# Kernel tuning notes

Measured on AMD Instinct MI355X. Metric: run time of the kernel, lower is better.

## Reference

```python
import jax, jax.numpy as jnp
import numpy as np

N_VERTS = 1_000_000
N_EDGES = 3_000_000
H, W = 1024, 1024
MAX_DEPTH = 10.0
DEPTH_SCALE = 1.0
CREGU = 2000.0


def setup_inputs() -> dict:
    key = jax.random.key(0)
    k1, k2, k3, k4, k5, k6 = jax.random.split(key, 6)
    # mesh vertices roughly in a unit-radius blob
    vertices = jax.random.normal(k1, (N_VERTS, 3), dtype=jnp.float32) * 0.5
    vertices_ref = vertices + 0.01 * jax.random.normal(k2, (N_VERTS, 3), dtype=jnp.float32)
    quaternion = jax.random.normal(k3, (4,), dtype=jnp.float32) + jnp.array([0., 0., 0., 1.], jnp.float32)
    translation = jax.random.normal(k4, (3,), dtype=jnp.float32) * 0.05
    hand_image = jax.random.uniform(k5, (H, W), dtype=jnp.float32) * MAX_DEPTH
    # camera per MeshDepthFitterEnergy.setImage: R = diag(1,-1,-1), focal = 2*W
    object_center = np.zeros(3, np.float32)
    object_radius = 0.5
    camera_center = object_center + np.array([-0.5, 0.0, 5.0], np.float32) * object_radius
    R = np.array([[1., 0., 0.], [0., -1., 0.], [0., 0., -1.]], np.float32)
    T = -R.T.dot(camera_center)
    focal = 2.0 * W
    intrinsic = jnp.array([[focal, 0., W / 2.], [0., focal, H / 2.], [0., 0., 1.]], jnp.float32)
    extrinsic = jnp.array(np.column_stack((R, T)), jnp.float32)
    edges = jax.random.randint(k6, (N_EDGES, 2), 0, N_VERTS, dtype=jnp.int64)
    return {"vertices": vertices, "vertices_ref": vertices_ref, "quaternion": quaternion,
            "translation": translation, "hand_image": hand_image,
            "intrinsic": intrinsic, "extrinsic": extrinsic, "edges": edges}


def _qrot(q, v):
    # q: [4] (x,y,z,w) normalized; v: [N,3]
    qvec = q[:3]
    uv = jnp.cross(jnp.broadcast_to(qvec, v.shape), v)
    uuv = jnp.cross(jnp.broadcast_to(qvec, v.shape), uv)
    return v + 2.0 * (q[3] * uv + uuv)


def _forward(vertices, vertices_ref, quaternion, translation, hand_image,
             intrinsic, extrinsic, edges):
    # rigid transform
    q = quaternion / jnp.linalg.norm(quaternion)
    v_centered = vertices - jnp.mean(vertices, axis=0, keepdims=True)
    v_t = _qrot(q, v_centered) + translation  # [N,3]
    # camera projection: P_cam = R x + T ; pix = K P_cam / z
    p_cam = v_t @ extrinsic[:, :3].T + extrinsic[:, 3]  # [N,3]
    proj = p_cam @ intrinsic.T
    z = p_cam[:, 2] * DEPTH_SCALE
    u = proj[:, 0] / proj[:, 2]
    v = proj[:, 1] / proj[:, 2]
    xi = jnp.clip(jnp.round(u), 0, W - 1).astype(jnp.int32)
    yi = jnp.clip(jnp.round(v), 0, H - 1).astype(jnp.int32)
    flat = yi * W + xi  # [N]
    # z-buffer: scatter-min of per-vertex depth (invalid/behind-camera -> MAX_DEPTH)
    zvalid = jnp.where(z > 0, z, MAX_DEPTH)
    depth_flat = jnp.full((H * W,), MAX_DEPTH, dtype=vertices.dtype).at[flat].min(zvalid)
    depth = jnp.clip(depth_flat, 0.0, MAX_DEPTH).reshape(H, W)
    diff_image = (depth - hand_image) ** 2
    e_data = jnp.sum(diff_image)
    # Laplacian rigid energy: cregu * || L (V - Vref) ||^2 over the edge graph
    dv = vertices - vertices_ref
    src, dst = edges[:, 0], edges[:, 1]
    deg = jax.ops.segment_sum(jnp.ones((N_EDGES,), vertices.dtype), src, num_segments=N_VERTS)
    neigh = jax.ops.segment_sum(dv[dst], src, num_segments=N_VERTS)  # [N,3]
    ldv = deg[:, None] * dv - neigh
    e_rigid = CREGU * jnp.sum(ldv ** 2)
    return e_data + e_rigid


def reference(vertices, vertices_ref, quaternion, translation, hand_image,
              intrinsic, extrinsic, edges):
    return _forward(vertices, vertices_ref, quaternion, translation, hand_image,
                    intrinsic, extrinsic, edges)
```

## Files before the change

### kernel.cpp

```cpp
#include <hip/hip_runtime.h>

#define W_IMG 1024
#define H_IMG 1024
#define HW_IMG (W_IMG * H_IMG)
#define NV 1000000
#define NE 3000000
#define NV4 (NE / 2)
#define MAX_DEPTH 10.0f
#define CREGU 2000.0f

#define NBUCKET 245
#define BSHIFT 12
#define BSIZE 4096
#define CAPSHIFT 14
#define CAP (1 << CAPSHIFT)

#define PREP_BLOCKS 2048
#define SCAT_V4 2048
#define SCAT_EDGES (SCAT_V4 * 2)
#define SCAT_BLOCKS ((NV4 + SCAT_V4 - 1) / SCAT_V4)
#define GEO_BLOCKS 2048
#define TSIZE 1024
#define EB 1024
#define EDATA_BLOCKS 64

#define QXY 4096.0f
#define IQXY 2.44140625e-4f
#define QZ 2048.0f
#define IQZ 4.8828125e-4f
#define BXY2 1024
#define BZ2 512

typedef int v4i __attribute__((ext_vector_type(4)));
typedef unsigned v4u __attribute__((ext_vector_type(4)));

__device__ __forceinline__ unsigned pack_dv32(float x, float y, float z) {
    x = fminf(fmaxf(x, -0.2f), 0.2f);
    y = fminf(fmaxf(y, -0.2f), 0.2f);
    z = fminf(fmaxf(z, -0.2f), 0.2f);
    unsigned px = (unsigned)((int)rintf(x * QXY) + BXY2);
    unsigned py = (unsigned)((int)rintf(y * QXY) + BXY2);
    unsigned pz = (unsigned)((int)rintf(z * QZ) + BZ2);
    return (px << 21) | (py << 10) | pz;
}

__device__ __forceinline__ unsigned long long expand_dv(unsigned p) {
    unsigned long long x = (p >> 21) & 0x7FFu;
    unsigned long long y = (p >> 10) & 0x7FFu;
    unsigned long long z = p & 0x3FFu;
    return (x << 44) | (y << 24) | (z << 6) | 1ull;
}

__device__ __forceinline__ float block_sum(float v, float* smem) {
#pragma unroll
    for (int o = 32; o > 0; o >>= 1) v += __shfl_down(v, o, 64);
    int lane = threadIdx.x & 63;
    int wid  = threadIdx.x >> 6;
    int nw   = blockDim.x >> 6;
    if (lane == 0) smem[wid] = v;
    __syncthreads();
    float r = 0.f;
    if (threadIdx.x == 0)
        for (int w = 0; w < nw; ++w) r += smem[w];
    __syncthreads();
    return r;
}

__device__ __forceinline__ void prefix245_fast(const unsigned* __restrict__ src,
                                               unsigned* dst, unsigned* wtmp) {
    int t = threadIdx.x;
    int lane = t & 63, wid = t >> 6;
    unsigned h = (t < NBUCKET) ? src[t] : 0u;
    unsigned incl = h;
#pragma unroll
    for (int o = 1; o < 64; o <<= 1) {
        unsigned v = __shfl_up(incl, o, 64);
        if (lane >= o) incl += v;
    }
    if (lane == 63) wtmp[wid] = incl;
    __syncthreads();
    unsigned woff = 0u;
    if (wid > 0) woff += wtmp[0];
    if (wid > 1) woff += wtmp[1];
    if (wid > 2) woff += wtmp[2];
    dst[t] = woff + incl - h;
    __syncthreads();
}

struct ScatSM {
    unsigned sort[SCAT_EDGES];
    unsigned char sBin[SCAT_EDGES];
    unsigned sLh[NBUCKET];
    unsigned sPfx[256];
    unsigned sDelta[256];
    unsigned wtmp[4];
};

__global__ void k_prep(const float* __restrict__ verts,
                       const float* __restrict__ verts_ref,
                       unsigned* __restrict__ pdv32,
                       unsigned* __restrict__ depth_bits, int ncd,
                       unsigned long long* __restrict__ neigh, int modeA,
                       const v4i* __restrict__ edges2,
                       unsigned* __restrict__ rec32,
                       unsigned* __restrict__ reserve,
                       float4* __restrict__ partial) {
    __shared__ float smem[4];
    __shared__ ScatSM sc;

    if (blockIdx.x < SCAT_BLOCKS) {
        if (!modeA) return;
        int base = blockIdx.x * SCAT_V4;
        for (int t = threadIdx.x; t < NBUCKET; t += blockDim.x) sc.sLh[t] = 0u;
        __syncthreads();

        v4i e[8];
        unsigned r0[8], r1[8];
#pragma unroll
        for (int k = 0; k < 8; ++k) {
            int idx = base + k * 256 + (int)threadIdx.x;
            if (idx < NV4) {
                e[k] = __builtin_nontemporal_load(&edges2[idx]);
                r0[k] = atomicAdd(&sc.sLh[(unsigned)e[k].x >> BSHIFT], 1u);
                r1[k] = atomicAdd(&sc.sLh[(unsigned)e[k].z >> BSHIFT], 1u);
            }
        }
        __syncthreads();
        prefix245_fast(sc.sLh, sc.sPfx, sc.wtmp);
        for (int t = threadIdx.x; t < NBUCKET; t += blockDim.x) {
            unsigned c = sc.sLh[t];
            unsigned res = c ? atomicAdd(&reserve[t], c) : 0u;
            sc.sDelta[t] = ((unsigned)t << CAPSHIFT) + res - sc.sPfx[t];
        }
#pragma unroll
        for (int k = 0; k < 8; ++k) {
            int idx = base + k * 256 + (int)threadIdx.x;
            if (idx < NV4) {
                unsigned s0 = (unsigned)e[k].x;
                unsigned b0 = s0 >> BSHIFT;
                unsigned slot0 = sc.sPfx[b0] + r0[k];
                sc.sort[slot0] = ((unsigned)e[k].y << 12) | (s0 & (BSIZE - 1));
                sc.sBin[slot0] = (unsigned char)b0;
                unsigned s1 = (unsigned)e[k].z;
                unsigned b1 = s1 >> BSHIFT;
                unsigned slot1 = sc.sPfx[b1] + r1[k];
                sc.sort[slot1] = ((unsigned)e[k].w << 12) | (s1 & (BSIZE - 1));
                sc.sBin[slot1] = (unsigned char)b1;
            }
        }
        __syncthreads();
        int nrec = (base + SCAT_V4 <= NV4) ? SCAT_EDGES : 2 * (NV4 - base);
#pragma unroll
        for (int k = 0; k < 16; ++k) {
            int t = k * 256 + (int)threadIdx.x;
            if (t < nrec) {
                unsigned r = sc.sort[t];
                unsigned b = sc.sBin[t];
                unsigned g = t + sc.sDelta[b];
                if (g - ((unsigned)b << CAPSHIFT) < CAP)
                    rec32[g] = r;
            }
        }
        return;
    }

    int sid = blockIdx.x - SCAT_BLOCKS;
    int i = sid * blockDim.x + threadIdx.x;
    int stride = PREP_BLOCKS * blockDim.x;

    float sx = 0.f, sy = 0.f, sz = 0.f;
    for (int j = i; j < NV; j += stride) {
        float x = verts[3 * j + 0];
        float y = verts[3 * j + 1];
        float z = verts[3 * j + 2];
        sx += x; sy += y; sz += z;
        pdv32[j] = pack_dv32(x - verts_ref[3 * j + 0],
                             y - verts_ref[3 * j + 1],
                             z - verts_ref[3 * j + 2]);
        if (!modeA) neigh[j] = 0ull;
    }

    size_t totd4 = (size_t)ncd * (HW_IMG / 4);
    v4u dinit;
    dinit.x = dinit.y = dinit.z = dinit.w = 0x41200000u;
    for (size_t j = i; j < totd4; j += stride) ((v4u*)depth_bits)[j] = dinit;

    float bx = block_sum(sx, smem);
    float by = block_sum(sy, smem);
    float bz = block_sum(sz, smem);
    if (threadIdx.x == 0) {
        float4 p; p.x = bx; p.y = by; p.z = bz; p.w = 0.f;
        partial[sid] = p;
    }
}

__global__ void k_main(const v4i* __restrict__ edges2,
                       const unsigned* __restrict__ pdv32,
                       unsigned long long* __restrict__ neigh,
                       const float* __restrict__ verts,
                       const float* __restrict__ quat,
                       const float* __restrict__ trans,
                       const float* __restrict__ intr,
                       const float* __restrict__ extr,
                       const float4* __restrict__ partial,
                       unsigned* __restrict__ depth_bits, int ncd) {
    __shared__ struct {
        unsigned h_key[TSIZE];
        unsigned h_val[TSIZE];
        float rsm[8];
    } sm;

    if (blockIdx.x >= GEO_BLOCKS) {
        int sb = blockIdx.x - GEO_BLOCKS;
        int base = sb * SCAT_V4;
#pragma unroll
        for (int k = 0; k < 8; ++k) {
            int idx = base + k * 256 + (int)threadIdx.x;
            if (idx < NV4) {
                v4i e = __builtin_nontemporal_load(&edges2[idx]);
                atomicAdd(&neigh[(size_t)(unsigned)e.x], expand_dv(pdv32[e.y]));
                atomicAdd(&neigh[(size_t)(unsigned)e.z], expand_dv(pdv32[e.w]));
            }
        }
        return;
    }

    int gb = blockIdx.x;
    for (int s = threadIdx.x; s < TSIZE; s += blockDim.x) {
        sm.h_key[s] = 0xFFFFFFFFu;
        sm.h_val[s] = 0xFFFFFFFFu;
    }
    __syncthreads();

    float sx = 0.f, sy = 0.f, sz = 0.f;
    for (int p = threadIdx.x; p < PREP_BLOCKS; p += blockDim.x) {
        float4 v = partial[p];
        sx += v.x; sy += v.y; sz += v.z;
    }
    float bx = block_sum(sx, sm.rsm);
    float by = block_sum(sy, sm.rsm);
    float bz = block_sum(sz, sm.rsm);
    if (threadIdx.x == 0) {
        const float inv_nv = 1.0f / (float)NV;
        sm.rsm[4] = bx * inv_nv;
        sm.rsm[5] = by * inv_nv;
        sm.rsm[6] = bz * inv_nv;
    }
    __syncthreads();
    float mx = sm.rsm[4], my = sm.rsm[5], mz = sm.rsm[6];

    float qx = quat[0], qy = quat[1], qz = quat[2], qw = quat[3];
    float qn = rsqrtf(qx * qx + qy * qy + qz * qz + qw * qw);
    qx *= qn; qy *= qn; qz *= qn; qw *= qn;
    float t0 = trans[0], t1 = trans[1], t2 = trans[2];
    float e0 = extr[0], e1 = extr[1], e2 = extr[2],  e3 = extr[3];
    float e4 = extr[4], e5 = extr[5], e6 = extr[6],  e7 = extr[7];
    float e8 = extr[8], e9 = extr[9], e10 = extr[10], e11 = extr[11];
    float i0 = intr[0], i1 = intr[1], i2 = intr[2];
    float i3 = intr[3], i4 = intr[4], i5 = intr[5];
    float i6 = intr[6], i7 = intr[7], i8 = intr[8];

    unsigned* __restrict__ db = depth_bits + (size_t)(gb & (ncd - 1)) * HW_IMG;

    int stride = GEO_BLOCKS * blockDim.x;
    for (int j = gb * blockDim.x + threadIdx.x; j < NV; j += stride) {
        float vx = __builtin_nontemporal_load(&verts[3 * j + 0]) - mx;
        float vy = __builtin_nontemporal_load(&verts[3 * j + 1]) - my;
        float vz = __builtin_nontemporal_load(&verts[3 * j + 2]) - mz;

        float uvx = qy * vz - qz * vy;
        float uvy = qz * vx - qx * vz;
        float uvz = qx * vy - qy * vx;
        float uuvx = qy * uvz - qz * uvy;
        float uuvy = qz * uvx - qx * uvz;
        float uuvz = qx * uvy - qy * uvx;
        float tx = vx + 2.f * (qw * uvx + uuvx) + t0;
        float ty = vy + 2.f * (qw * uvy + uuvy) + t1;
        float tz = vz + 2.f * (qw * uvz + uuvz) + t2;

        float px = e0 * tx + e1 * ty + e2  * tz + e3;
        float py = e4 * tx + e5 * ty + e6  * tz + e7;
        float pz = e8 * tx + e9 * ty + e10 * tz + e11;

        float pr0 = i0 * px + i1 * py + i2 * pz;
        float pr1 = i3 * px + i4 * py + i5 * pz;
        float pr2 = i6 * px + i7 * py + i8 * pz;

        float u = pr0 / pr2;
        float v = pr1 / pr2;
        float ru = rintf(u);
        float rv = rintf(v);
        bool border = (ru < 0.f) | (ru > (float)(W_IMG - 1)) |
                      (rv < 0.f) | (rv > (float)(H_IMG - 1));
        float xf = fminf(fmaxf(ru, 0.f), (float)(W_IMG - 1));
        float yf = fminf(fmaxf(rv, 0.f), (float)(H_IMG - 1));
        unsigned flat = (unsigned)((int)yf * W_IMG + (int)xf);

        if (pz > 0.f) {
            unsigned zbits = __float_as_uint(pz);
            bool direct = !border;
            if (border) {
                unsigned slot = (flat * 2654435761u) >> 22;
                bool done = false;
#pragma unroll
                for (int p = 0; p < 4; ++p) {
                    unsigned old = atomicCAS(&sm.h_key[slot], 0xFFFFFFFFu, flat);
                    if (old == 0xFFFFFFFFu || old == flat) {
                        atomicMin(&sm.h_val[slot], zbits);
                        done = true;
                        break;
                    }
                    slot = (slot + 1) & (TSIZE - 1);
                }
                direct = !done;
            }
            if (direct) atomicMin(&db[flat], zbits);
        }
    }
    __syncthreads();
    for (int s = threadIdx.x; s < TSIZE; s += blockDim.x) {
        unsigned k = sm.h_key[s];
        if (k != 0xFFFFFFFFu) atomicMin(&db[k], sm.h_val[s]);
    }
}

__global__ __launch_bounds__(EB, 2)
void k_energy(const unsigned* __restrict__ depth_bits, int ncd,
              const float* __restrict__ hand,
              const unsigned* __restrict__ pdv32,
              const unsigned* __restrict__ rec32,
              const unsigned* __restrict__ reserve,
              const unsigned long long* __restrict__ neigh, int modeA,
              float* out) {
    __shared__ unsigned long long acc[BSIZE];
    __shared__ float smem[16];

    if (blockIdx.x < NBUCKET) {
        int b = blockIdx.x;
        int vbase = b * BSIZE;
        int nvert = (NV - vbase < BSIZE) ? (NV - vbase) : BSIZE;
        if (modeA) {
            unsigned count = reserve[b];
            if (count > CAP) count = CAP;
            const unsigned* rb = rec32 + ((size_t)b << CAPSHIFT);
            for (int v = threadIdx.x; v < BSIZE; v += blockDim.x) acc[v] = 0ull;
            __syncthreads();
            unsigned i = threadIdx.x;
            for (; i + 3u * EB < count; i += 4u * EB) {
                unsigned q0 = rb[i];
                unsigned q1 = rb[i + EB];
                unsigned q2 = rb[i + 2u * EB];
                unsigned q3 = rb[i + 3u * EB];
                unsigned p0 = pdv32[q0 >> 12];
                unsigned p1 = pdv32[q1 >> 12];
                unsigned p2 = pdv32[q2 >> 12];
                unsigned p3 = pdv32[q3 >> 12];
                atomicAdd(&acc[q0 & (BSIZE - 1u)], expand_dv(p0));
                atomicAdd(&acc[q1 & (BSIZE - 1u)], expand_dv(p1));
                atomicAdd(&acc[q2 & (BSIZE - 1u)], expand_dv(p2));
                atomicAdd(&acc[q3 & (BSIZE - 1u)], expand_dv(p3));
            }
            for (; i < count; i += EB) {
                unsigned q = rb[i];
                atomicAdd(&acc[q & (BSIZE - 1u)], expand_dv(pdv32[q >> 12]));
            }
            __syncthreads();
        }
        float lacc = 0.f;
        for (int v = threadIdx.x; v < nvert; v += blockDim.x) {
            unsigned long long n = modeA ? acc[v] : neigh[(size_t)vbase + v];
            int cnt = (int)(n & 63ull);
            int rz  = (int)((n >> 6)  & 0x3FFFFull);
            int ry  = (int)((n >> 24) & 0xFFFFFull);
            int rx  = (int)(n >> 44);
            float nx = (float)(rx - cnt * BXY2) * IQXY;
            float ny = (float)(ry - cnt * BXY2) * IQXY;
            float nz = (float)(rz - cnt * BZ2)  * IQZ;
            unsigned p = pdv32[vbase + v];
            float dx = (float)((int)((p >> 21) & 0x7FFu) - BXY2) * IQXY;
            float dy = (float)((int)((p >> 10) & 0x7FFu) - BXY2) * IQXY;
            float dz = (float)((int)(p & 0x3FFu) - BZ2) * IQZ;
            float dg = (float)cnt;
            float lx = dg * dx - nx;
            float ly = dg * dy - ny;
            float lz = dg * dz - nz;
            lacc += lx * lx + ly * ly + lz * lz;
        }
        float bsum = block_sum(lacc, smem);
        if (threadIdx.x == 0) atomicAdd(out, CREGU * bsum);
    } else {
        int eb = blockIdx.x - NBUCKET;
        int i = eb * blockDim.x + threadIdx.x;
        int stride = EDATA_BLOCKS * blockDim.x;
        float accd = 0.f;
        const int nq = HW_IMG / 4;
        for (int j = i; j < nq; j += stride) {
            v4u d0 = ((const v4u*)depth_bits)[j];
            float m0 = __uint_as_float(d0.x);
            float m1 = __uint_as_float(d0.y);
            float m2 = __uint_as_float(d0.z);
            float m3 = __uint_as_float(d0.w);
            for (int c = 1; c < ncd; ++c) {
                v4u dc = ((const v4u*)(depth_bits + (size_t)c * HW_IMG))[j];
                m0 = fminf(m0, __uint_as_float(dc.x));
                m1 = fminf(m1, __uint_as_float(dc.y));
                m2 = fminf(m2, __uint_as_float(dc.z));
                m3 = fminf(m3, __uint_as_float(dc.w));
            }
            const float* hp = hand + 4 * (size_t)j;
            float f0 = fminf(fmaxf(m0, 0.f), MAX_DEPTH) - hp[0];
            float f1 = fminf(fmaxf(m1, 0.f), MAX_DEPTH) - hp[1];
            float f2 = fminf(fmaxf(m2, 0.f), MAX_DEPTH) - hp[2];
            float f3 = fminf(fmaxf(m3, 0.f), MAX_DEPTH) - hp[3];
            accd += f0 * f0 + f1 * f1 + f2 * f2 + f3 * f3;
        }
        float bsum = block_sum(accd, smem);
        if (threadIdx.x == 0) atomicAdd(out, bsum);
    }
}

extern "C" void kernel_launch(void* const* d_in, const int* in_sizes, int n_in,
                              void* d_out, int out_size, void* d_ws, size_t ws_size,
                              hipStream_t stream) {
    const float* verts     = (const float*)d_in[0];
    const float* verts_ref = (const float*)d_in[1];
    const float* quat      = (const float*)d_in[2];
    const float* trans     = (const float*)d_in[3];
    const float* hand      = (const float*)d_in[4];
    const float* intr      = (const float*)d_in[5];
    const float* extr      = (const float*)d_in[6];
    const int*   edges     = (const int*)d_in[7];
    float* out = (float*)d_out;

    char* ws = (char*)d_ws;
    const size_t OFF_BINS = (size_t)NV * 4;
    const size_t OFF_PART = OFF_BINS + 4096;
    const size_t OFF_REC  = OFF_PART + (size_t)PREP_BLOCKS * 16;

    const size_t A_FIX = OFF_REC + ((size_t)NBUCKET << CAPSHIFT) * 4;
    const size_t B_FIX = OFF_REC + (size_t)NV * 8;

    int modeA, ncd;
    size_t OFF_DEPTH;
    if (ws_size >= A_FIX + 4ull * HW_IMG * 4)      { modeA = 1; ncd = 4; OFF_DEPTH = A_FIX; }
    else if (ws_size >= A_FIX + 2ull * HW_IMG * 4) { modeA = 1; ncd = 2; OFF_DEPTH = A_FIX; }
    else if (ws_size >= A_FIX + 1ull * HW_IMG * 4) { modeA = 1; ncd = 1; OFF_DEPTH = A_FIX; }
    else if (ws_size >= B_FIX + 4ull * HW_IMG * 4) { modeA = 0; ncd = 4; OFF_DEPTH = B_FIX; }
    else if (ws_size >= B_FIX + 2ull * HW_IMG * 4) { modeA = 0; ncd = 2; OFF_DEPTH = B_FIX; }
    else                                           { modeA = 0; ncd = 1; OFF_DEPTH = B_FIX; }

    unsigned*           pdv32      = (unsigned*)ws;
    unsigned*           hist       = (unsigned*)(ws + OFF_BINS);
    unsigned*           reserve    = hist + 256;
    float4*             partial    = (float4*)(ws + OFF_PART);
    unsigned*           rec32      = (unsigned*)(ws + OFF_REC);
    unsigned long long* neigh      = (unsigned long long*)(ws + OFF_REC);
    unsigned*           depth_bits = (unsigned*)(ws + OFF_DEPTH);

    const int B = 256;

    hipMemsetAsync(ws + OFF_BINS, 0, 4096, stream);
    hipMemsetAsync(d_out, 0, sizeof(float), stream);

    k_prep<<<SCAT_BLOCKS + PREP_BLOCKS, B, 0, stream>>>(
        verts, verts_ref, pdv32, depth_bits, ncd, neigh, modeA,
        (const v4i*)edges, rec32, reserve, partial);
    k_main<<<modeA ? GEO_BLOCKS : (GEO_BLOCKS + SCAT_BLOCKS), B, 0, stream>>>(
        (const v4i*)edges, pdv32, neigh,
        verts, quat, trans, intr, extr, partial, depth_bits, ncd);
    k_energy<<<NBUCKET + EDATA_BLOCKS, EB, 0, stream>>>(
        depth_bits, ncd, hand, pdv32, rec32, reserve, neigh, modeA, out);
}
```

Before: 214.7 us.

## Move bucketed neighbor accumulation into geometry kernel to overlap with rasterization

After: 201.5 us. 1.07x faster.

```diff
diff --git a/kernel.cpp b/kernel.cpp
--- a/kernel.cpp
+++ b/kernel.cpp
@@ -23,6 +23,7 @@
 #define TSIZE 1024
 #define EB 1024
 #define EDATA_BLOCKS 64
+#define EDATA_BLOCKS_A 128
 
 #define QXY 4096.0f
 #define IQXY 2.44140625e-4f
@@ -194,8 +195,22 @@
     }
 }
 
+union MainSM {
+    struct {
+        unsigned h_key[TSIZE];
+        unsigned h_val[TSIZE];
+        float rsm[8];
+    } geo;
+    struct {
+        unsigned long long acc[BSIZE];
+        float smem[4];
+    } bk;
+};
+
 __global__ void k_main(const v4i* __restrict__ edges2,
                        const unsigned* __restrict__ pdv32,
+                       const unsigned* __restrict__ rec32,
+                       const unsigned* __restrict__ reserve,
                        unsigned long long* __restrict__ neigh,
                        const float* __restrict__ verts,
                        const float* __restrict__ quat,
@@ -203,172 +218,42 @@
                        const float* __restrict__ intr,
                        const float* __restrict__ extr,
                        const float4* __restrict__ partial,
-                       unsigned* __restrict__ depth_bits, int ncd) {
-    __shared__ struct {
-        unsigned h_key[TSIZE];
-        unsigned h_val[TSIZE];
-        float rsm[8];
-    } sm;
-
-    if (blockIdx.x >= GEO_BLOCKS) {
-        int sb = blockIdx.x - GEO_BLOCKS;
-        int base = sb * SCAT_V4;
-#pragma unroll
-        for (int k = 0; k < 8; ++k) {
-            int idx = base + k * 256 + (int)threadIdx.x;
-            if (idx < NV4) {
-                v4i e = __builtin_nontemporal_load(&edges2[idx]);
-                atomicAdd(&neigh[(size_t)(unsigned)e.x], expand_dv(pdv32[e.y]));
-                atomicAdd(&neigh[(size_t)(unsigned)e.z], expand_dv(pdv32[e.w]));
-            }
-        }
-        return;
-    }
-
-    int gb = blockIdx.x;
-    for (int s = threadIdx.x; s < TSIZE; s += blockDim.x) {
-        sm.h_key[s] = 0xFFFFFFFFu;
-        sm.h_val[s] = 0xFFFFFFFFu;
-    }
-    __syncthreads();
-
-    float sx = 0.f, sy = 0.f, sz = 0.f;
-    for (int p = threadIdx.x; p < PREP_BLOCKS; p += blockDim.x) {
-        float4 v = partial[p];
-        sx += v.x; sy += v.y; sz += v.z;
-    }
-    float bx = block_sum(sx, sm.rsm);
-    float by = block_sum(sy, sm.rsm);
-    float bz = block_sum(sz, sm.rsm);
-    if (threadIdx.x == 0) {
-        const float inv_nv = 1.0f / (float)NV;
-        sm.rsm[4] = bx * inv_nv;
-        sm.rsm[5] = by * inv_nv;
-        sm.rsm[6] = bz * inv_nv;
-    }
-    __syncthreads();
-    float mx = sm.rsm[4], my = sm.rsm[5], mz = sm.rsm[6];
-
-    float qx = quat[0], qy = quat[1], qz = quat[2], qw = quat[3];
-    float qn = rsqrtf(qx * qx + qy * qy + qz * qz + qw * qw);
-    qx *= qn; qy *= qn; qz *= qn; qw *= qn;
-    float t0 = trans[0], t1 = trans[1], t2 = trans[2];
-    float e0 = extr[0], e1 = extr[1], e2 = extr[2],  e3 = extr[3];
-    float e4 = extr[4], e5 = extr[5], e6 = extr[6],  e7 = extr[7];
-    float e8 = extr[8], e9 = extr[9], e10 = extr[10], e11 = extr[11];
-    float i0 = intr[0], i1 = intr[1], i2 = intr[2];
-    float i3 = intr[3], i4 = intr[4], i5 = intr[5];
-    float i6 = intr[6], i7 = intr[7], i8 = intr[8];
-
-    unsigned* __restrict__ db = depth_bits + (size_t)(gb & (ncd - 1)) * HW_IMG;
-
-    int stride = GEO_BLOCKS * blockDim.x;
-    for (int j = gb * blockDim.x + threadIdx.x; j < NV; j += stride) {
-        float vx = __builtin_nontemporal_load(&verts[3 * j + 0]) - mx;
-        float vy = __builtin_nontemporal_load(&verts[3 * j + 1]) - my;
-        float vz = __builtin_nontemporal_load(&verts[3 * j + 2]) - mz;
-
-        float uvx = qy * vz - qz * vy;
-        float uvy = qz * vx - qx * vz;
-        float uvz = qx * vy - qy * vx;
-        float uuvx = qy * uvz - qz * uvy;
-        float uuvy = qz * uvx - qx * uvz;
-        float uuvz = qx * uvy - qy * uvx;
-        float tx = vx + 2.f * (qw * uvx + uuvx) + t0;
-        float ty = vy + 2.f * (qw * uvy + uuvy) + t1;
-        float tz = vz + 2.f * (qw * uvz + uuvz) + t2;
-
-        float px = e0 * tx + e1 * ty + e2  * tz + e3;
-        float py = e4 * tx + e5 * ty + e6  * tz + e7;
-        float pz = e8 * tx + e9 * ty + e10 * tz + e11;
-
-        float pr0 = i0 * px + i1 * py + i2 * pz;
-        float pr1 = i3 * px + i4 * py + i5 * pz;
-        float pr2 = i6 * px + i7 * py + i8 * pz;
-
-        float u = pr0 / pr2;
-        float v = pr1 / pr2;
-        float ru = rintf(u);
-        float rv = rintf(v);
-        bool border = (ru < 0.f) | (ru > (float)(W_IMG - 1)) |
-                      (rv < 0.f) | (rv > (float)(H_IMG - 1));
-        float xf = fminf(fmaxf(ru, 0.f), (float)(W_IMG - 1));
-        float yf = fminf(fmaxf(rv, 0.f), (float)(H_IMG - 1));
-        unsigned flat = (unsigned)((int)yf * W_IMG + (int)xf);
-
-        if (pz > 0.f) {
-            unsigned zbits = __float_as_uint(pz);
-            bool direct = !border;
-            if (border) {
-                unsigned slot = (flat * 2654435761u) >> 22;
-                bool done = false;
-#pragma unroll
-                for (int p = 0; p < 4; ++p) {
-                    unsigned old = atomicCAS(&sm.h_key[slot], 0xFFFFFFFFu, flat);
-                    if (old == 0xFFFFFFFFu || old == flat) {
-                        atomicMin(&sm.h_val[slot], zbits);
-                        done = true;
-                        break;
-                    }
-                    slot = (slot + 1) & (TSIZE - 1);
-                }
-                direct = !done;
-            }
-            if (direct) atomicMin(&db[flat], zbits);
-        }
-    }
-    __syncthreads();
-    for (int s = threadIdx.x; s < TSIZE; s += blockDim.x) {
-        unsigned k = sm.h_key[s];
-        if (k != 0xFFFFFFFFu) atomicMin(&db[k], sm.h_val[s]);
-    }
-}
-
-__global__ __launch_bounds__(EB, 2)
-void k_energy(const unsigned* __restrict__ depth_bits, int ncd,
-              const float* __restrict__ hand,
-              const unsigned* __restrict__ pdv32,
-              const unsigned* __restrict__ rec32,
-              const unsigned* __restrict__ reserve,
-              const unsigned long long* __restrict__ neigh, int modeA,
-              float* out) {
-    __shared__ unsigned long long acc[BSIZE];
-    __shared__ float smem[16];
-
-    if (blockIdx.x < NBUCKET) {
+                       unsigned* __restrict__ depth_bits, int ncd,
+                       int nb, float* __restrict__ out) {
+    __shared__ MainSM sm;
+
+    if ((int)blockIdx.x < nb) {
         int b = blockIdx.x;
         int vbase = b * BSIZE;
         int nvert = (NV - vbase < BSIZE) ? (NV - vbase) : BSIZE;
-        if (modeA) {
-            unsigned count = reserve[b];
-            if (count > CAP) count = CAP;
-            const unsigned* rb = rec32 + ((size_t)b << CAPSHIFT);
-            for (int v = threadIdx.x; v < BSIZE; v += blockDim.x) acc[v] = 0ull;
-            __syncthreads();
-            unsigned i = threadIdx.x;
-            for (; i + 3u * EB < count; i += 4u * EB) {
-                unsigned q0 = rb[i];
-                unsigned q1 = rb[i + EB];
-                unsigned q2 = rb[i + 2u * EB];
-                unsigned q3 = rb[i + 3u * EB];
-                unsigned p0 = pdv32[q0 >> 12];
-                unsigned p1 = pdv32[q1 >> 12];
-                unsigned p2 = pdv32[q2 >> 12];
-                unsigned p3 = pdv32[q3 >> 12];
-                atomicAdd(&acc[q0 & (BSIZE - 1u)], expand_dv(p0));
-                atomicAdd(&acc[q1 & (BSIZE - 1u)], expand_dv(p1));
-                atomicAdd(&acc[q2 & (BSIZE - 1u)], expand_dv(p2));
-                atomicAdd(&acc[q3 & (BSIZE - 1u)], expand_dv(p3));
-            }
-            for (; i < count; i += EB) {
-                unsigned q = rb[i];
-                atomicAdd(&acc[q & (BSIZE - 1u)], expand_dv(pdv32[q >> 12]));
-            }
-            __syncthreads();
-        }
+        unsigned count = reserve[b];
+        if (count > CAP) count = CAP;
+        const unsigned* rb = rec32 + ((size_t)b << CAPSHIFT);
+        for (int v = threadIdx.x; v < BSIZE; v += blockDim.x) sm.bk.acc[v] = 0ull;
+        __syncthreads();
+        unsigned i = threadIdx.x;
+        for (; i + 768u < count; i += 1024u) {
+            unsigned q0 = rb[i];
+            unsigned q1 = rb[i + 256u];
+            unsigned q2 = rb[i + 512u];
+            unsigned q3 = rb[i + 768u];
+            unsigned p0 = pdv32[q0 >> 12];
+            unsigned p1 = pdv32[q1 >> 12];
+            unsigned p2 = pdv32[q2 >> 12];
+            unsigned p3 = pdv32[q3 >> 12];
+            atomicAdd(&sm.bk.acc[q0 & (BSIZE - 1u)], expand_dv(p0));
+            atomicAdd(&sm.bk.acc[q1 & (BSIZE - 1u)], expand_dv(p1));
+            atomicAdd(&sm.bk.acc[q2 & (BSIZE - 1u)], expand_dv(p2));
+            atomicAdd(&sm.bk.acc[q3 & (BSIZE - 1u)], expand_dv(p3));
+        }
+        for (; i < count; i += 256u) {
+            unsigned q = rb[i];
+            atomicAdd(&sm.bk.acc[q & (BSIZE - 1u)], expand_dv(pdv32[q >> 12]));
+        }
+        __syncthreads();
         float lacc = 0.f;
         for (int v = threadIdx.x; v < nvert; v += blockDim.x) {
-            unsigned long long n = modeA ? acc[v] : neigh[(size_t)vbase + v];
+            unsigned long long n = sm.bk.acc[v];
             int cnt = (int)(n & 63ull);
             int rz  = (int)((n >> 6)  & 0x3FFFFull);
             int ry  = (int)((n >> 24) & 0xFFFFFull);
@@ -386,12 +271,164 @@
             float lz = dg * dz - nz;
             lacc += lx * lx + ly * ly + lz * lz;
         }
+        float bsum = block_sum(lacc, sm.bk.smem);
+        if (threadIdx.x == 0) atomicAdd(out, CREGU * bsum);
+        return;
+    }
+
+    int gb = blockIdx.x - nb;
+    if (gb >= GEO_BLOCKS) {
+        int sb = gb - GEO_BLOCKS;
+        int base = sb * SCAT_V4;
+#pragma unroll
+        for (int k = 0; k < 8; ++k) {
+            int idx = base + k * 256 + (int)threadIdx.x;
+            if (idx < NV4) {
+                v4i e = __builtin_nontemporal_load(&edges2[idx]);
+                atomicAdd(&neigh[(size_t)(unsigned)e.x], expand_dv(pdv32[e.y]));
+                atomicAdd(&neigh[(size_t)(unsigned)e.z], expand_dv(pdv32[e.w]));
+            }
+        }
+        return;
+    }
+
+    for (int s = threadIdx.x; s < TSIZE; s += blockDim.x) {
+        sm.geo.h_key[s] = 0xFFFFFFFFu;
+        sm.geo.h_val[s] = 0xFFFFFFFFu;
+    }
+    __syncthreads();
+
+    float sx = 0.f, sy = 0.f, sz = 0.f;
+    for (int p = threadIdx.x; p < PREP_BLOCKS; p += blockDim.x) {
+        float4 v = partial[p];
+        sx += v.x; sy += v.y; sz += v.z;
+    }
+    float bx = block_sum(sx, sm.geo.rsm);
+    float by = block_sum(sy, sm.geo.rsm);
+    float bz = block_sum(sz, sm.geo.rsm);
+    if (threadIdx.x == 0) {
+        const float inv_nv = 1.0f / (float)NV;
+        sm.geo.rsm[4] = bx * inv_nv;
+        sm.geo.rsm[5] = by * inv_nv;
+        sm.geo.rsm[6] = bz * inv_nv;
+    }
+    __syncthreads();
+    float mx = sm.geo.rsm[4], my = sm.geo.rsm[5], mz = sm.geo.rsm[6];
+
+    float qx = quat[0], qy = quat[1], qz = quat[2], qw = quat[3];
+    float qn = rsqrtf(qx * qx + qy * qy + qz * qz + qw * qw);
+    qx *= qn; qy *= qn; qz *= qn; qw *= qn;
+    float t0 = trans[0], t1 = trans[1], t2 = trans[2];
+    float e0 = extr[0], e1 = extr[1], e2 = extr[2],  e3 = extr[3];
+    float e4 = extr[4], e5 = extr[5], e6 = extr[6],  e7 = extr[7];
+    float e8 = extr[8], e9 = extr[9], e10 = extr[10], e11 = extr[11];
+    float i0 = intr[0], i1 = intr[1], i2 = intr[2];
+    float i3 = intr[3], i4 = intr[4], i5 = intr[5];
+    float i6 = intr[6], i7 = intr[7], i8 = intr[8];
+
+    unsigned* __restrict__ db = depth_bits + (size_t)(gb & (ncd - 1)) * HW_IMG;
+
+    int stride = GEO_BLOCKS * blockDim.x;
+    for (int j = gb * blockDim.x + threadIdx.x; j < NV; j += stride) {
+        float vx = __builtin_nontemporal_load(&verts[3 * j + 0]) - mx;
+        float vy = __builtin_nontemporal_load(&verts[3 * j + 1]) - my;
+        float vz = __builtin_nontemporal_load(&verts[3 * j + 2]) - mz;
+
+        float uvx = qy * vz - qz * vy;
+        float uvy = qz * vx - qx * vz;
+        float uvz = qx * vy - qy * vx;
+        float uuvx = qy * uvz - qz * uvy;
+        float uuvy = qz * uvx - qx * uvz;
+        float uuvz = qx * uvy - qy * uvx;
+        float tx = vx + 2.f * (qw * uvx + uuvx) + t0;
+        float ty = vy + 2.f * (qw * uvy + uuvy) + t1;
+        float tz = vz + 2.f * (qw * uvz + uuvz) + t2;
+
+        float px = e0 * tx + e1 * ty + e2  * tz + e3;
+        float py = e4 * tx + e5 * ty + e6  * tz + e7;
+        float pz = e8 * tx + e9 * ty + e10 * tz + e11;
+
+        float pr0 = i0 * px + i1 * py + i2 * pz;
+        float pr1 = i3 * px + i4 * py + i5 * pz;
+        float pr2 = i6 * px + i7 * py + i8 * pz;
+
+        float u = pr0 / pr2;
+        float v = pr1 / pr2;
+        float ru = rintf(u);
+        float rv = rintf(v);
+        bool border = (ru < 0.f) | (ru > (float)(W_IMG - 1)) |
+                      (rv < 0.f) | (rv > (float)(H_IMG - 1));
+        float xf = fminf(fmaxf(ru, 0.f), (float)(W_IMG - 1));
+        float yf = fminf(fmaxf(rv, 0.f), (float)(H_IMG - 1));
+        unsigned flat = (unsigned)((int)yf * W_IMG + (int)xf);
+
+        if (pz > 0.f) {
+            unsigned zbits = __float_as_uint(pz);
+            bool direct = !border;
+            if (border) {
+                unsigned slot = (flat * 2654435761u) >> 22;
+                bool done = false;
+#pragma unroll
+                for (int p = 0; p < 4; ++p) {
+                    unsigned old = atomicCAS(&sm.geo.h_key[slot], 0xFFFFFFFFu, flat);
+                    if (old == 0xFFFFFFFFu || old == flat) {
+                        atomicMin(&sm.geo.h_val[slot], zbits);
+                        done = true;
+                        break;
+                    }
+                    slot = (slot + 1) & (TSIZE - 1);
+                }
+                direct = !done;
+            }
+            if (direct) atomicMin(&db[flat], zbits);
+        }
+    }
+    __syncthreads();
+    for (int s = threadIdx.x; s < TSIZE; s += blockDim.x) {
+        unsigned k = sm.geo.h_key[s];
+        if (k != 0xFFFFFFFFu) atomicMin(&db[k], sm.geo.h_val[s]);
+    }
+}
+
+__global__ __launch_bounds__(EB, 2)
+void k_energy(const unsigned* __restrict__ depth_bits, int ncd,
+              const float* __restrict__ hand,
+              const unsigned* __restrict__ pdv32,
+              const unsigned long long* __restrict__ neigh, int nbk,
+              float* out) {
+    __shared__ float smem[16];
+
+    if ((int)blockIdx.x < nbk) {
+        int b = blockIdx.x;
+        int vbase = b * BSIZE;
+        int nvert = (NV - vbase < BSIZE) ? (NV - vbase) : BSIZE;
+        float lacc = 0.f;
+        for (int v = threadIdx.x; v < nvert; v += blockDim.x) {
+            unsigned long long n = neigh[(size_t)vbase + v];
+            int cnt = (int)(n & 63ull);
+            int rz  = (int)((n >> 6)  & 0x3FFFFull);
+            int ry  = (int)((n >> 24) & 0xFFFFFull);
+            int rx  = (int)(n >> 44);
+            float nx = (float)(rx - cnt * BXY2) * IQXY;
+            float ny = (float)(ry - cnt * BXY2) * IQXY;
+            float nz = (float)(rz - cnt * BZ2)  * IQZ;
+            unsigned p = pdv32[vbase + v];
+            float dx = (float)((int)((p >> 21) & 0x7FFu) - BXY2) * IQXY;
+            float dy = (float)((int)((p >> 10) & 0x7FFu) - BXY2) * IQXY;
+            float dz = (float)((int)(p & 0x3FFu) - BZ2) * IQZ;
+            float dg = (float)cnt;
+            float lx = dg * dx - nx;
+            float ly = dg * dy - ny;
+            float lz = dg * dz - nz;
+            lacc += lx * lx + ly * ly + lz * lz;
+        }
         float bsum = block_sum(lacc, smem);
         if (threadIdx.x == 0) atomicAdd(out, CREGU * bsum);
     } else {
-        int eb = blockIdx.x - NBUCKET;
+        int eb = blockIdx.x - nbk;
+        int nedb = gridDim.x - nbk;
         int i = eb * blockDim.x + threadIdx.x;
-        int stride = EDATA_BLOCKS * blockDim.x;
+        int stride = nedb * blockDim.x;
         float accd = 0.f;
         const int nq = HW_IMG / 4;
         for (int j = i; j < nq; j += stride) {
@@ -465,9 +502,15 @@
     k_prep<<<SCAT_BLOCKS + PREP_BLOCKS, B, 0, stream>>>(
         verts, verts_ref, pdv32, depth_bits, ncd, neigh, modeA,
         (const v4i*)edges, rec32, reserve, partial);
-    k_main<<<modeA ? GEO_BLOCKS : (GEO_BLOCKS + SCAT_BLOCKS), B, 0, stream>>>(
-        (const v4i*)edges, pdv32, neigh,
-        verts, quat, trans, intr, extr, partial, depth_bits, ncd);
-    k_energy<<<NBUCKET + EDATA_BLOCKS, EB, 0, stream>>>(
-        depth_bits, ncd, hand, pdv32, rec32, reserve, neigh, modeA, out);
-}
+
+    int nb = modeA ? NBUCKET : 0;
+    int main_grid = modeA ? (NBUCKET + GEO_BLOCKS) : (GEO_BLOCKS + SCAT_BLOCKS);
+    k_main<<<main_grid, B, 0, stream>>>(
+        (const v4i*)edges, pdv32, rec32, reserve, neigh,
+        verts, quat, trans, intr, extr, partial, depth_bits, ncd, nb, out);
+
+    int nbk = modeA ? 0 : NBUCKET;
+    int en_grid = modeA ? EDATA_BLOCKS_A : (NBUCKET + EDATA_BLOCKS);
+    k_energy<<<en_grid, EB, 0, stream>>>(
+        depth_bits, ncd, hand, pdv32, neigh, nbk, out);
+}
```

## Move edge bucket-scatter into main kernel alongside projection, drop memset

Applied to the files above, without the earlier changes.

New measurement: 204.5 us. 1.05x faster.

```diff
diff --git a/kernel.cpp b/kernel.cpp
--- a/kernel.cpp
+++ b/kernel.cpp
@@ -23,6 +23,7 @@
 #define TSIZE 1024
 #define EB 1024
 #define EDATA_BLOCKS 64
+#define EDATA_BLOCKS_A 128
 
 #define QXY 4096.0f
 #define IQXY 2.44140625e-4f
@@ -87,86 +88,18 @@
     __syncthreads();
 }
 
-struct ScatSM {
-    unsigned sort[SCAT_EDGES];
-    unsigned char sBin[SCAT_EDGES];
-    unsigned sLh[NBUCKET];
-    unsigned sPfx[256];
-    unsigned sDelta[256];
-    unsigned wtmp[4];
-};
-
 __global__ void k_prep(const float* __restrict__ verts,
                        const float* __restrict__ verts_ref,
                        unsigned* __restrict__ pdv32,
                        unsigned* __restrict__ depth_bits, int ncd,
                        unsigned long long* __restrict__ neigh, int modeA,
-                       const v4i* __restrict__ edges2,
-                       unsigned* __restrict__ rec32,
-                       unsigned* __restrict__ reserve,
-                       float4* __restrict__ partial) {
+                       float4* __restrict__ partial,
+                       float* __restrict__ out) {
     __shared__ float smem[4];
-    __shared__ ScatSM sc;
-
-    if (blockIdx.x < SCAT_BLOCKS) {
-        if (!modeA) return;
-        int base = blockIdx.x * SCAT_V4;
-        for (int t = threadIdx.x; t < NBUCKET; t += blockDim.x) sc.sLh[t] = 0u;
-        __syncthreads();
-
-        v4i e[8];
-        unsigned r0[8], r1[8];
-#pragma unroll
-        for (int k = 0; k < 8; ++k) {
-            int idx = base + k * 256 + (int)threadIdx.x;
-            if (idx < NV4) {
-                e[k] = __builtin_nontemporal_load(&edges2[idx]);
-                r0[k] = atomicAdd(&sc.sLh[(unsigned)e[k].x >> BSHIFT], 1u);
-                r1[k] = atomicAdd(&sc.sLh[(unsigned)e[k].z >> BSHIFT], 1u);
-            }
-        }
-        __syncthreads();
-        prefix245_fast(sc.sLh, sc.sPfx, sc.wtmp);
-        for (int t = threadIdx.x; t < NBUCKET; t += blockDim.x) {
-            unsigned c = sc.sLh[t];
-            unsigned res = c ? atomicAdd(&reserve[t], c) : 0u;
-            sc.sDelta[t] = ((unsigned)t << CAPSHIFT) + res - sc.sPfx[t];
-        }
-#pragma unroll
-        for (int k = 0; k < 8; ++k) {
-            int idx = base + k * 256 + (int)threadIdx.x;
-            if (idx < NV4) {
-                unsigned s0 = (unsigned)e[k].x;
-                unsigned b0 = s0 >> BSHIFT;
-                unsigned slot0 = sc.sPfx[b0] + r0[k];
-                sc.sort[slot0] = ((unsigned)e[k].y << 12) | (s0 & (BSIZE - 1));
-                sc.sBin[slot0] = (unsigned char)b0;
-                unsigned s1 = (unsigned)e[k].z;
-                unsigned b1 = s1 >> BSHIFT;
-                unsigned slot1 = sc.sPfx[b1] + r1[k];
-                sc.sort[slot1] = ((unsigned)e[k].w << 12) | (s1 & (BSIZE - 1));
-                sc.sBin[slot1] = (unsigned char)b1;
-            }
-        }
-        __syncthreads();
-        int nrec = (base + SCAT_V4 <= NV4) ? SCAT_EDGES : 2 * (NV4 - base);
-#pragma unroll
-        for (int k = 0; k < 16; ++k) {
-            int t = k * 256 + (int)threadIdx.x;
-            if (t < nrec) {
-                unsigned r = sc.sort[t];
-                unsigned b = sc.sBin[t];
-                unsigned g = t + sc.sDelta[b];
-                if (g - ((unsigned)b << CAPSHIFT) < CAP)
-                    rec32[g] = r;
-            }
-        }
-        return;
-    }
-
-    int sid = blockIdx.x - SCAT_BLOCKS;
-    int i = sid * blockDim.x + threadIdx.x;
-    int stride = PREP_BLOCKS * blockDim.x;
+    int i = blockIdx.x * blockDim.x + threadIdx.x;
+    int stride = gridDim.x * blockDim.x;
+
+    if (i == 0) *out = 0.f;
 
     float sx = 0.f, sy = 0.f, sz = 0.f;
     for (int j = i; j < NV; j += stride) {
@@ -190,13 +123,33 @@
     float bz = block_sum(sz, smem);
     if (threadIdx.x == 0) {
         float4 p; p.x = bx; p.y = by; p.z = bz; p.w = 0.f;
-        partial[sid] = p;
-    }
-}
+        partial[blockIdx.x] = p;
+    }
+}
+
+struct ScatSM {
+    unsigned sort[SCAT_EDGES];
+    unsigned char sBin[SCAT_EDGES];
+    unsigned sLh[NBUCKET];
+    unsigned sPfx[256];
+    unsigned sDelta[256];
+    unsigned wtmp[4];
+};
+
+union MainSM {
+    ScatSM sc;
+    struct {
+        unsigned h_key[TSIZE];
+        unsigned h_val[TSIZE];
+        float rsm[8];
+    } geo;
+};
 
 __global__ void k_main(const v4i* __restrict__ edges2,
                        const unsigned* __restrict__ pdv32,
-                       unsigned long long* __restrict__ neigh,
+                       unsigned* __restrict__ rec32,
+                       unsigned* __restrict__ reserve,
+                       unsigned long long* __restrict__ neigh, int modeA,
                        const float* __restrict__ verts,
                        const float* __restrict__ quat,
                        const float* __restrict__ trans,
@@ -204,31 +157,79 @@
                        const float* __restrict__ extr,
                        const float4* __restrict__ partial,
                        unsigned* __restrict__ depth_bits, int ncd) {
-    __shared__ struct {
-        unsigned h_key[TSIZE];
-        unsigned h_val[TSIZE];
-        float rsm[8];
-    } sm;
-
-    if (blockIdx.x >= GEO_BLOCKS) {
-        int sb = blockIdx.x - GEO_BLOCKS;
-        int base = sb * SCAT_V4;
-#pragma unroll
-        for (int k = 0; k < 8; ++k) {
-            int idx = base + k * 256 + (int)threadIdx.x;
-            if (idx < NV4) {
-                v4i e = __builtin_nontemporal_load(&edges2[idx]);
-                atomicAdd(&neigh[(size_t)(unsigned)e.x], expand_dv(pdv32[e.y]));
-                atomicAdd(&neigh[(size_t)(unsigned)e.z], expand_dv(pdv32[e.w]));
+    __shared__ MainSM sm;
+
+    if (blockIdx.x < SCAT_BLOCKS) {
+        int base = blockIdx.x * SCAT_V4;
+        if (modeA) {
+            for (int t = threadIdx.x; t < NBUCKET; t += blockDim.x) sm.sc.sLh[t] = 0u;
+            __syncthreads();
+
+            v4i e[8];
+            unsigned r0[8], r1[8];
+#pragma unroll
+            for (int k = 0; k < 8; ++k) {
+                int idx = base + k * 256 + (int)threadIdx.x;
+                if (idx < NV4) {
+                    e[k] = __builtin_nontemporal_load(&edges2[idx]);
+                    r0[k] = atomicAdd(&sm.sc.sLh[(unsigned)e[k].x >> BSHIFT], 1u);
+                    r1[k] = atomicAdd(&sm.sc.sLh[(unsigned)e[k].z >> BSHIFT], 1u);
+                }
+            }
+            __syncthreads();
+            prefix245_fast(sm.sc.sLh, sm.sc.sPfx, sm.sc.wtmp);
+            for (int t = threadIdx.x; t < NBUCKET; t += blockDim.x) {
+                unsigned c = sm.sc.sLh[t];
+                unsigned res = c ? atomicAdd(&reserve[t], c) : 0u;
+                sm.sc.sDelta[t] = ((unsigned)t << CAPSHIFT) + res - sm.sc.sPfx[t];
+            }
+#pragma unroll
+            for (int k = 0; k < 8; ++k) {
+                int idx = base + k * 256 + (int)threadIdx.x;
+                if (idx < NV4) {
+                    unsigned s0 = (unsigned)e[k].x;
+                    unsigned b0 = s0 >> BSHIFT;
+                    unsigned slot0 = sm.sc.sPfx[b0] + r0[k];
+                    sm.sc.sort[slot0] = ((unsigned)e[k].y << 12) | (s0 & (BSIZE - 1));
+                    sm.sc.sBin[slot0] = (unsigned char)b0;
+                    unsigned s1 = (unsigned)e[k].z;
+                    unsigned b1 = s1 >> BSHIFT;
+                    unsigned slot1 = sm.sc.sPfx[b1] + r1[k];
+                    sm.sc.sort[slot1] = ((unsigned)e[k].w << 12) | (s1 & (BSIZE - 1));
+                    sm.sc.sBin[slot1] = (unsigned char)b1;
+                }
+            }
+            __syncthreads();
+            int nrec = (base + SCAT_V4 <= NV4) ? SCAT_EDGES : 2 * (NV4 - base);
+#pragma unroll
+            for (int k = 0; k < 16; ++k) {
+                int t = k * 256 + (int)threadIdx.x;
+                if (t < nrec) {
+                    unsigned r = sm.sc.sort[t];
+                    unsigned b = sm.sc.sBin[t];
+                    unsigned g = t + sm.sc.sDelta[b];
+                    if (g - ((unsigned)b << CAPSHIFT) < CAP)
+                        rec32[g] = r;
+                }
+            }
+        } else {
+#pragma unroll
+            for (int k = 0; k < 8; ++k) {
+                int idx = base + k * 256 + (int)threadIdx.x;
+                if (idx < NV4) {
+                    v4i e = __builtin_nontemporal_load(&edges2[idx]);
+                    atomicAdd(&neigh[(size_t)(unsigned)e.x], expand_dv(pdv32[e.y]));
+                    atomicAdd(&neigh[(size_t)(unsigned)e.z], expand_dv(pdv32[e.w]));
+                }
             }
         }
         return;
     }
 
-    int gb = blockIdx.x;
+    int gb = blockIdx.x - SCAT_BLOCKS;
     for (int s = threadIdx.x; s < TSIZE; s += blockDim.x) {
-        sm.h_key[s] = 0xFFFFFFFFu;
-        sm.h_val[s] = 0xFFFFFFFFu;
+        sm.geo.h_key[s] = 0xFFFFFFFFu;
+        sm.geo.h_val[s] = 0xFFFFFFFFu;
     }
     __syncthreads();
 
@@ -237,17 +238,17 @@
         float4 v = partial[p];
         sx += v.x; sy += v.y; sz += v.z;
     }
-    float bx = block_sum(sx, sm.rsm);
-    float by = block_sum(sy, sm.rsm);
-    float bz = block_sum(sz, sm.rsm);
+    float bx = block_sum(sx, sm.geo.rsm);
+    float by = block_sum(sy, sm.geo.rsm);
+    float bz = block_sum(sz, sm.geo.rsm);
     if (threadIdx.x == 0) {
         const float inv_nv = 1.0f / (float)NV;
-        sm.rsm[4] = bx * inv_nv;
-        sm.rsm[5] = by * inv_nv;
-        sm.rsm[6] = bz * inv_nv;
-    }
-    __syncthreads();
-    float mx = sm.rsm[4], my = sm.rsm[5], mz = sm.rsm[6];
+        sm.geo.rsm[4] = bx * inv_nv;
+        sm.geo.rsm[5] = by * inv_nv;
+        sm.geo.rsm[6] = bz * inv_nv;
+    }
+    __syncthreads();
+    float mx = sm.geo.rsm[4], my = sm.geo.rsm[5], mz = sm.geo.rsm[6];
 
     float qx = quat[0], qy = quat[1], qz = quat[2], qw = quat[3];
     float qn = rsqrtf(qx * qx + qy * qy + qz * qz + qw * qw);
@@ -264,9 +265,9 @@
 
     int stride = GEO_BLOCKS * blockDim.x;
     for (int j = gb * blockDim.x + threadIdx.x; j < NV; j += stride) {
-        float vx = __builtin_nontemporal_load(&verts[3 * j + 0]) - mx;
-        float vy = __builtin_nontemporal_load(&verts[3 * j + 1]) - my;
-        float vz = __builtin_nontemporal_load(&verts[3 * j + 2]) - mz;
+        float vx = verts[3 * j + 0] - mx;
+        float vy = verts[3 * j + 1] - my;
+        float vz = verts[3 * j + 2] - mz;
 
         float uvx = qy * vz - qz * vy;
         float uvy = qz * vx - qx * vz;
@@ -304,9 +305,9 @@
                 bool done = false;
 #pragma unroll
                 for (int p = 0; p < 4; ++p) {
-                    unsigned old = atomicCAS(&sm.h_key[slot], 0xFFFFFFFFu, flat);
+                    unsigned old = atomicCAS(&sm.geo.h_key[slot], 0xFFFFFFFFu, flat);
                     if (old == 0xFFFFFFFFu || old == flat) {
-                        atomicMin(&sm.h_val[slot], zbits);
+                        atomicMin(&sm.geo.h_val[slot], zbits);
                         done = true;
                         break;
                     }
@@ -319,8 +320,8 @@
     }
     __syncthreads();
     for (int s = threadIdx.x; s < TSIZE; s += blockDim.x) {
-        unsigned k = sm.h_key[s];
-        if (k != 0xFFFFFFFFu) atomicMin(&db[k], sm.h_val[s]);
+        unsigned k = sm.geo.h_key[s];
+        if (k != 0xFFFFFFFFu) atomicMin(&db[k], sm.geo.h_val[s]);
     }
 }
 
@@ -335,7 +336,7 @@
     __shared__ unsigned long long acc[BSIZE];
     __shared__ float smem[16];
 
-    if (blockIdx.x < NBUCKET) {
+    if ((int)blockIdx.x < NBUCKET) {
         int b = blockIdx.x;
         int vbase = b * BSIZE;
         int nvert = (NV - vbase < BSIZE) ? (NV - vbase) : BSIZE;
@@ -390,8 +391,9 @@
         if (threadIdx.x == 0) atomicAdd(out, CREGU * bsum);
     } else {
         int eb = blockIdx.x - NBUCKET;
+        int nedb = gridDim.x - NBUCKET;
         int i = eb * blockDim.x + threadIdx.x;
-        int stride = EDATA_BLOCKS * blockDim.x;
+        int stride = nedb * blockDim.x;
         float accd = 0.f;
         const int nq = HW_IMG / 4;
         for (int j = i; j < nq; j += stride) {
@@ -460,14 +462,15 @@
     const int B = 256;
 
     hipMemsetAsync(ws + OFF_BINS, 0, 4096, stream);
-    hipMemsetAsync(d_out, 0, sizeof(float), stream);
-
-    k_prep<<<SCAT_BLOCKS + PREP_BLOCKS, B, 0, stream>>>(
-        verts, verts_ref, pdv32, depth_bits, ncd, neigh, modeA,
-        (const v4i*)edges, rec32, reserve, partial);
-    k_main<<<modeA ? GEO_BLOCKS : (GEO_BLOCKS + SCAT_BLOCKS), B, 0, stream>>>(
-        (const v4i*)edges, pdv32, neigh,
+
+    k_prep<<<PREP_BLOCKS, B, 0, stream>>>(
+        verts, verts_ref, pdv32, depth_bits, ncd, neigh, modeA, partial, out);
+
+    k_main<<<SCAT_BLOCKS + GEO_BLOCKS, B, 0, stream>>>(
+        (const v4i*)edges, pdv32, rec32, reserve, neigh, modeA,
         verts, quat, trans, intr, extr, partial, depth_bits, ncd);
-    k_energy<<<NBUCKET + EDATA_BLOCKS, EB, 0, stream>>>(
+
+    int en_grid = modeA ? (NBUCKET + EDATA_BLOCKS_A) : (NBUCKET + EDATA_BLOCKS);
+    k_energy<<<en_grid, EB, 0, stream>>>(
         depth_bits, ncd, hand, pdv32, rec32, reserve, neigh, modeA, out);
 }
```
